# Kernel optimization log

Hardware: AMD Instinct MI355X
Metric: run time of the kernel (lower is better)

## Reference

```python
import jax, jax.numpy as jnp
import numpy as np

EPS = 1e-6
HEADS, HEAD_DIM = 8, 64

def rms_norm_ch(x, g):
    # x: [B,C,H,W], normalize over channel dim, scale g: [C]
    mean = jnp.mean(x * x, axis=1, keepdims=True)
    return x * jax.lax.rsqrt(mean + EPS) * g[None, :, None, None]

def rms_norm_last(x, g):
    # x: [B,L,D], normalize over feature dim, scale g: [D]
    mean = jnp.mean(x * x, axis=-1, keepdims=True)
    return x * jax.lax.rsqrt(mean + EPS) * g

def setup_inputs() -> dict:
    key = jax.random.key(0)
    ks = jax.random.split(key, 5)
    B, C, H, W = 8, 512, 32, 32
    Lc = 1024
    hidden = HEADS * HEAD_DIM  # 512
    x = jax.random.normal(ks[0], (B, C, H, W), dtype=jnp.float32)
    context = jax.random.normal(ks[1], (B, Lc, C), dtype=jnp.float32)
    Wq = jax.random.normal(ks[2], (hidden, C), dtype=jnp.float32) * 0.02
    Wkv = jax.random.normal(ks[3], (2 * hidden, C), dtype=jnp.float32) * 0.02
    Wo = jax.random.normal(ks[4], (C, hidden), dtype=jnp.float32) * 0.02
    bo = jnp.zeros((C,), dtype=jnp.float32)
    g = jnp.ones((C,), dtype=jnp.float32)   # shared RMSNorm scale (pre-attn)
    g2 = jnp.ones((C,), dtype=jnp.float32)  # output RMSNorm scale
    return {"x": x, "context": context, "Wq": Wq, "Wkv": Wkv, "Wo": Wo, "bo": bo, "g": g, "g2": g2}

def reference(x, context, Wq, Wkv, Wo, bo, g, g2):
    B, C, H, W = x.shape
    Lc = context.shape[1]
    hidden = HEADS * HEAD_DIM
    scale = HEAD_DIM ** -0.5

    # Q projection: 1x1 conv == per-pixel matmul
    xn = rms_norm_ch(x, g)
    q = jnp.einsum('oc,bchw->bohw', Wq, xn)                     # [B,hidden,H,W]
    q = q.reshape(B, HEADS, HEAD_DIM, H * W) * scale            # [B,h,d,lw1]

    # K,V from context tokens
    cn = rms_norm_last(context, g)
    kv = jnp.einsum('bld,od->blo', cn, Wkv)                     # [B,Lc,2*hidden]
    k, v = jnp.split(kv, 2, axis=-1)
    k = k.reshape(B, Lc, HEADS, HEAD_DIM).transpose(0, 2, 3, 1)  # [B,h,d,lw2]
    v = v.reshape(B, Lc, HEADS, HEAD_DIM).transpose(0, 2, 3, 1)  # [B,h,d,lw2]

    sim = jnp.einsum('bhci,bhcj->bhij', q, k)                   # [B,h,lw1,lw2]
    attn = jax.nn.softmax(sim, axis=-1)
    out = jnp.einsum('bhij,bhcj->bhic', attn, v)                # [B,h,lw1,d]

    out = out.transpose(0, 1, 3, 2).reshape(B, hidden, H, W)    # b (h c) l w
    y = jnp.einsum('oc,bchw->bohw', Wo, out) + bo[None, :, None, None]
    y = rms_norm_ch(y, g2)
    return y + x
```

## Files before the change

kernel.cpp:

```cpp
#include <hip/hip_runtime.h>
#include <hip/hip_bf16.h>

using bf16 = __hip_bfloat16;
typedef float f32x4 __attribute__((ext_vector_type(4)));
typedef short s16x8 __attribute__((ext_vector_type(8)));
typedef short s16x4 __attribute__((ext_vector_type(4)));

#define B_N   8
#define C_N   512
#define HW_N  1024
#define LC_N  1024
#define HID_N 512
#define NHEAD 8
#define DHEAD 64
#define EPSN  1e-6f

__device__ __forceinline__ f32x4 mfma16(s16x8 a, s16x8 b, f32x4 c) {
  return __builtin_amdgcn_mfma_f32_16x16x32_bf16(a, b, c, 0, 0, 0);
}
__device__ __forceinline__ void gload_lds16(const void* g, void* l) {
  __builtin_amdgcn_global_load_lds((const __attribute__((address_space(1))) void*)g,
                                   (__attribute__((address_space(3))) void*)l, 16, 0, 0);
}
__device__ __forceinline__ s16x8 ld8(const bf16* p) {
  return *reinterpret_cast<const s16x8*>(p);
}
__device__ __forceinline__ unsigned short bfbits(float f) {
  return __builtin_bit_cast(unsigned short, __float2bfloat16(f));
}

__global__ __launch_bounds__(256) void prep_weights(
    const float* __restrict__ Wq, const float* __restrict__ Wkv,
    const float* __restrict__ Wo, const float* __restrict__ g,
    bf16* __restrict__ Wqg, bf16* __restrict__ Wkvg, bf16* __restrict__ Wob,
    float* __restrict__ ssq)
{
  int idx = blockIdx.x * 256 + threadIdx.x;
  const int NQ = 512 * 512, NKV = 1024 * 512;
  if (idx < 8192) ssq[idx] = 0.f;
  if (idx < NQ) {
    Wqg[idx] = __float2bfloat16(Wq[idx] * g[idx & 511]);
  } else if (idx < NQ + NKV) {
    int j = idx - NQ;
    Wkvg[j] = __float2bfloat16(Wkv[j] * g[j & 511]);
  } else {
    int j = idx - NQ - NKV;
    Wob[j] = __float2bfloat16(Wo[j]);
  }
}

__global__ __launch_bounds__(256) void rstd_ch_kernel(
    const float* __restrict__ x, float* __restrict__ rstd)
{
  __shared__ float part[16][16];
  int tp = threadIdx.x & 15, tc = threadIdx.x >> 4;
  int gp = blockIdx.x * 16 + tp;
  int b = gp >> 10, p = gp & 1023;
  const float* xb = x + (long)b * C_N * HW_N + p;
  float s = 0.f;
  for (int c = tc * 32; c < tc * 32 + 32; ++c) {
    float v = xb[(long)c * HW_N];
    s += v * v;
  }
  part[tc][tp] = s;
  __syncthreads();
  if (tc == 0) {
    float tot = 0.f;
#pragma unroll
    for (int i = 0; i < 16; ++i) tot += part[i][tp];
    rstd[gp] = rsqrtf(tot * (1.0f / C_N) + EPSN);
  }
}

__global__ __launch_bounds__(256) void xbf_kernel(
    const float* __restrict__ x, const float* __restrict__ rstd, bf16* __restrict__ xbf)
{
  __shared__ float tile[32][33];
  int b = blockIdx.z, c0 = blockIdx.y * 32, p0 = blockIdx.x * 32;
  int tx = threadIdx.x & 31, ty = threadIdx.x >> 5;
#pragma unroll
  for (int j = 0; j < 4; ++j) {
    int c = ty + j * 8;
    tile[c][tx] = x[((long)b * C_N + c0 + c) * HW_N + p0 + tx];
  }
  __syncthreads();
#pragma unroll
  for (int j = 0; j < 4; ++j) {
    int p = ty + j * 8;
    float r = rstd[b * HW_N + p0 + p];
    xbf[((long)b * HW_N + p0 + p) * C_N + c0 + tx] = __float2bfloat16(tile[tx][p] * r);
  }
}

__global__ __launch_bounds__(256) void ctxnorm_kernel(
    const float* __restrict__ ctx, bf16* __restrict__ cnbf)
{
  int row = blockIdx.x * 4 + (threadIdx.x >> 6);
  int lane = threadIdx.x & 63;
  const float* cr = ctx + (long)row * C_N;
  float4 v0 = ((const float4*)cr)[lane * 2];
  float4 v1 = ((const float4*)cr)[lane * 2 + 1];
  float s = v0.x*v0.x + v0.y*v0.y + v0.z*v0.z + v0.w*v0.w
          + v1.x*v1.x + v1.y*v1.y + v1.z*v1.z + v1.w*v1.w;
#pragma unroll
  for (int m = 1; m < 64; m <<= 1) s += __shfl_xor(s, m);
  float r = rsqrtf(s * (1.0f / C_N) + EPSN);
  bf16 tmp[8];
  tmp[0] = __float2bfloat16(v0.x * r); tmp[1] = __float2bfloat16(v0.y * r);
  tmp[2] = __float2bfloat16(v0.z * r); tmp[3] = __float2bfloat16(v0.w * r);
  tmp[4] = __float2bfloat16(v1.x * r); tmp[5] = __float2bfloat16(v1.y * r);
  tmp[6] = __float2bfloat16(v1.z * r); tmp[7] = __float2bfloat16(v1.w * r);
  *reinterpret_cast<s16x8*>(cnbf + (long)row * C_N + lane * 8) =
      *reinterpret_cast<const s16x8*>(tmp);
}

__device__ __forceinline__ void gemm128_core(
    const bf16* __restrict__ A, const bf16* __restrict__ W, int K, int m0, int n0,
    bf16* __restrict__ sA, bf16* __restrict__ sB, f32x4 (&acc)[4][4])
{
  const int t = threadIdx.x;
  const int lane = t & 63, w = t >> 6;
  const int wm = (w >> 1) * 64, wn = (w & 1) * 64;
  const int lr = lane & 15, hi = lane >> 4;
  const int r = t >> 2, seg = t & 3;
  const long aoff0 = (long)(m0 + r) * K + seg * 8;
  const long aoff1 = (long)(m0 + 64 + r) * K + seg * 8;
  const long woff0 = (long)(n0 + r) * K + seg * 8;
  const long woff1 = (long)(n0 + 64 + r) * K + seg * 8;
  const int d0 = r * 32 + seg * 8, d1 = (64 + r) * 32 + seg * 8;

#define GSTAGE(buf, k0)                                           \
  do {                                                            \
    gload_lds16(A + aoff0 + (k0), &sA[(buf) * 4096 + d0]);        \
    gload_lds16(A + aoff1 + (k0), &sA[(buf) * 4096 + d1]);        \
    gload_lds16(W + woff0 + (k0), &sB[(buf) * 4096 + d0]);        \
    gload_lds16(W + woff1 + (k0), &sB[(buf) * 4096 + d1]);        \
  } while (0)

  GSTAGE(0, 0);
  __syncthreads();
  int cur = 0;
  for (int k0 = 0; k0 < K; k0 += 32) {
    if (k0 + 32 < K) GSTAGE(cur ^ 1, k0 + 32);
    s16x8 af[4], bfr[4];
#pragma unroll
    for (int mi = 0; mi < 4; ++mi)
      af[mi] = *reinterpret_cast<const s16x8*>(
          &sA[cur * 4096 + (wm + mi * 16 + lr) * 32 + hi * 8]);
#pragma unroll
    for (int ni = 0; ni < 4; ++ni)
      bfr[ni] = *reinterpret_cast<const s16x8*>(
          &sB[cur * 4096 + (wn + ni * 16 + lr) * 32 + hi * 8]);
#pragma unroll
    for (int mi = 0; mi < 4; ++mi)
#pragma unroll
      for (int ni = 0; ni < 4; ++ni)
        acc[mi][ni] = mfma16(af[mi], bfr[ni], acc[mi][ni]);
    __syncthreads();
    cur ^= 1;
  }
#undef GSTAGE
}

__global__ __launch_bounds__(256, 2)
void gemm_qkv(const bf16* __restrict__ xbf, const bf16* __restrict__ cnbf,
              const bf16* __restrict__ Wqg, const bf16* __restrict__ Wkvg,
              bf16* __restrict__ qbf, bf16* __restrict__ kvbf, bf16* __restrict__ vT)
{
  __shared__ bf16 sA[2 * 4096];
  __shared__ bf16 sB[2 * 4096];
  const int bid = blockIdx.x;
  const bf16 *A, *W;
  int N, m0, n0;
  bool isQ;
  if (bid < 256) {
    isQ = true;  A = xbf;  W = Wqg;  N = HID_N;
    m0 = (bid >> 2) * 128; n0 = (bid & 3) * 128;
  } else {
    isQ = false; A = cnbf; W = Wkvg; N = 2 * HID_N;
    int b2 = bid - 256;
    m0 = (b2 >> 3) * 128; n0 = (b2 & 7) * 128;
  }
  f32x4 acc[4][4] = {};
  gemm128_core(A, W, C_N, m0, n0, sA, sB, acc);

  const int lane = threadIdx.x & 63, w = threadIdx.x >> 6;
  const int wm = (w >> 1) * 64, wn = (w & 1) * 64;
  const int lr = lane & 15, hi = lane >> 4;
  const float scale = isQ ? 0.18033688011112042f : 1.0f;
#pragma unroll
  for (int mi = 0; mi < 4; ++mi) {
#pragma unroll
    for (int ni = 0; ni < 4; ++ni) {
#pragma unroll
      for (int rr = 0; rr < 4; ++rr) {
        int row = m0 + wm + mi * 16 + hi * 4 + rr;
        int col = n0 + wn + ni * 16 + lr;
        float v = acc[mi][ni][rr] * scale;
        if (isQ) {
          qbf[(long)row * HID_N + col] = __float2bfloat16(v);
        } else if (col < HID_N) {
          kvbf[(long)row * (2 * HID_N) + col] = __float2bfloat16(v);
        } else {
          int b = row >> 10, l = row & 1023;
          vT[((long)b * HID_N + (col - HID_N)) * LC_N + l] = __float2bfloat16(v);
        }
      }
    }
  }
}

__global__ __launch_bounds__(256, 2)
void gemm_o(const bf16* __restrict__ attno, const bf16* __restrict__ Wob,
            const float* __restrict__ bo, float* __restrict__ ytmp,
            float* __restrict__ ssq)
{
  __shared__ bf16 sA[2 * 4096];
  __shared__ bf16 sB[2 * 4096];
  const int m0 = (blockIdx.x >> 2) * 128;
  const int n0 = (blockIdx.x & 3) * 128;
  f32x4 acc[4][4] = {};
  gemm128_core(attno, Wob, HID_N, m0, n0, sA, sB, acc);

  const int lane = threadIdx.x & 63, w = threadIdx.x >> 6;
  const int wm = (w >> 1) * 64, wn = (w & 1) * 64;
  const int lr = lane & 15, hi = lane >> 4;
  float ss[4][4];
#pragma unroll
  for (int mi = 0; mi < 4; ++mi)
#pragma unroll
    for (int rr = 0; rr < 4; ++rr) ss[mi][rr] = 0.f;

#pragma unroll
  for (int mi = 0; mi < 4; ++mi) {
#pragma unroll
    for (int ni = 0; ni < 4; ++ni) {
      float bb = bo[n0 + wn + ni * 16 + lr];
#pragma unroll
      for (int rr = 0; rr < 4; ++rr) {
        int row = m0 + wm + mi * 16 + hi * 4 + rr;
        int col = n0 + wn + ni * 16 + lr;
        float v = acc[mi][ni][rr] + bb;
        ytmp[(long)row * C_N + col] = v;
        ss[mi][rr] += v * v;
      }
    }
  }
#pragma unroll
  for (int mi = 0; mi < 4; ++mi)
#pragma unroll
    for (int rr = 0; rr < 4; ++rr) {
      float s = ss[mi][rr];
      s += __shfl_xor(s, 1); s += __shfl_xor(s, 2);
      s += __shfl_xor(s, 4); s += __shfl_xor(s, 8);
      if (lr == 0) atomicAdd(&ssq[m0 + wm + mi * 16 + hi * 4 + rr], s);
    }
}

__global__ __launch_bounds__(256, 2)
void attn_fused(const bf16* __restrict__ qbf, const bf16* __restrict__ kvbf,
                const bf16* __restrict__ vT, bf16* __restrict__ attno)
{
  __shared__ bf16 sK[2][4096];
  __shared__ bf16 sV[2][4096];
  __shared__ bf16 Pl[4][32 * 72];
  const int t = threadIdx.x;
  const int wv = t >> 6, lane = t & 63;
  const int lr = lane & 15, hi = lane >> 4;
  const int hi8 = hi * 8, hi4 = hi * 4;
  const int bh = blockIdx.x, b = bh >> 3, h = bh & 7;
  const int q_base = blockIdx.y * 128 + wv * 32;

  const bf16* kbase = kvbf + (long)b * LC_N * 1024 + h * DHEAD;
  const bf16* vbase = vT + ((long)b * HID_N + h * DHEAD) * (long)LC_N;
  bf16* Pw = Pl[wv];

  s16x8 qf[2][2];
#pragma unroll
  for (int qt = 0; qt < 2; ++qt)
#pragma unroll
    for (int c = 0; c < 2; ++c)
      qf[qt][c] = ld8(qbf + ((long)b * HW_N + q_base + qt * 16 + lr) * HID_N
                          + h * DHEAD + c * 32 + hi8);

  const int srow = lane >> 2;
  const int scol = (lane & 3) * 8;

#define ASTAGE(buf, l0n)                                                        \
  do {                                                                          \
    _Pragma("unroll")                                                           \
    for (int j = 0; j < 4; ++j) {                                               \
      int lin = wv * 4 + j;                                                     \
      int cc = (lin >> 2) & 1, qq = lin & 3;                                    \
      if (lin < 8) {                                                            \
        gload_lds16(kbase + (long)((l0n) + qq * 16 + srow) * 1024 + cc * 32 + scol, \
                    &sK[buf][cc * 2048 + qq * 512 + lane * 8]);                 \
      } else {                                                                  \
        gload_lds16(vbase + (long)(qq * 16 + srow) * 1024 + (l0n) + cc * 32 + scol, \
                    &sV[buf][cc * 2048 + qq * 512 + lane * 8]);                 \
      }                                                                         \
    }                                                                           \
  } while (0)

  float m[2] = {-1e30f, -1e30f};
  float lsum[2] = {0.f, 0.f};
  f32x4 o[2][4] = {};

  ASTAGE(0, 0);
  __syncthreads();
  int cur = 0;

#pragma unroll 1
  for (int l0 = 0; l0 < LC_N; l0 += 64) {
    if (l0 + 64 < LC_N) ASTAGE(cur ^ 1, l0 + 64);

    f32x4 st[4][2] = {};
#pragma unroll
    for (int kt = 0; kt < 4; ++kt) {
      s16x8 k0 = *reinterpret_cast<const s16x8*>(&sK[cur][(kt * 16 + lr) * 32 + hi8]);
      s16x8 k1 = *reinterpret_cast<const s16x8*>(&sK[cur][2048 + (kt * 16 + lr) * 32 + hi8]);
      st[kt][0] = mfma16(k0, qf[0][0], st[kt][0]);
      st[kt][0] = mfma16(k1, qf[0][1], st[kt][0]);
      st[kt][1] = mfma16(k0, qf[1][0], st[kt][1]);
      st[kt][1] = mfma16(k1, qf[1][1], st[kt][1]);
    }

    float pmax[2];
#pragma unroll
    for (int qt = 0; qt < 2; ++qt) {
      float mx = st[0][qt][0];
#pragma unroll
      for (int kt = 0; kt < 4; ++kt)
#pragma unroll
        for (int rr = 0; rr < 4; ++rr)
          mx = fmaxf(mx, st[kt][qt][rr]);
      pmax[qt] = mx;
    }
    bool ok = (pmax[0] <= m[0] + 8.f) && (pmax[1] <= m[1] + 8.f);
    if (!__all(ok)) {
#pragma unroll
      for (int qt = 0; qt < 2; ++qt) {
        float rm = pmax[qt];
        rm = fmaxf(rm, __shfl_xor(rm, 16));
        rm = fmaxf(rm, __shfl_xor(rm, 32));
        float mn = fmaxf(m[qt], rm);
        float al = __builtin_amdgcn_exp2f(m[qt] - mn);
        m[qt] = mn;
        lsum[qt] *= al;
        float arr[4];
#pragma unroll
        for (int rr = 0; rr < 4; ++rr) arr[rr] = __shfl(al, hi4 + rr);
#pragma unroll
        for (int dt = 0; dt < 4; ++dt)
#pragma unroll
          for (int rr = 0; rr < 4; ++rr) o[qt][dt][rr] *= arr[rr];
      }
    }

#pragma unroll
    for (int qt = 0; qt < 2; ++qt) {
      float ls = 0.f;
#pragma unroll
      for (int kt = 0; kt < 4; ++kt) {
        float p0 = __builtin_amdgcn_exp2f(st[kt][qt][0] - m[qt]);
        float p1 = __builtin_amdgcn_exp2f(st[kt][qt][1] - m[qt]);
        float p2 = __builtin_amdgcn_exp2f(st[kt][qt][2] - m[qt]);
        float p3 = __builtin_amdgcn_exp2f(st[kt][qt][3] - m[qt]);
        ls += (p0 + p1) + (p2 + p3);
        s16x4 pk;
        pk[0] = (short)bfbits(p0); pk[1] = (short)bfbits(p1);
        pk[2] = (short)bfbits(p2); pk[3] = (short)bfbits(p3);
        *reinterpret_cast<s16x4*>(&Pw[(qt * 16 + lr) * 72 + kt * 16 + hi4]) = pk;
      }
      lsum[qt] += ls;
    }

#pragma unroll
    for (int c = 0; c < 2; ++c) {
      s16x8 pa0 = *reinterpret_cast<const s16x8*>(&Pw[(0 * 16 + lr) * 72 + c * 32 + hi8]);
      s16x8 pa1 = *reinterpret_cast<const s16x8*>(&Pw[(1 * 16 + lr) * 72 + c * 32 + hi8]);
#pragma unroll
      for (int dt = 0; dt < 4; ++dt) {
        s16x8 vv = *reinterpret_cast<const s16x8*>(
            &sV[cur][c * 2048 + (dt * 16 + lr) * 32 + hi8]);
        o[0][dt] = mfma16(pa0, vv, o[0][dt]);
        o[1][dt] = mfma16(pa1, vv, o[1][dt]);
      }
    }

    __syncthreads();
    cur ^= 1;
  }
#undef ASTAGE

#pragma unroll
  for (int qt = 0; qt < 2; ++qt) {
    float ls = lsum[qt];
    ls += __shfl_xor(ls, 16);
    ls += __shfl_xor(ls, 32);
    float linv[4];
#pragma unroll
    for (int rr = 0; rr < 4; ++rr) linv[rr] = 1.f / __shfl(ls, hi4 + rr);
#pragma unroll
    for (int dt = 0; dt < 4; ++dt)
#pragma unroll
      for (int rr = 0; rr < 4; ++rr)
        attno[((long)b * HW_N + q_base + qt * 16 + hi4 + rr) * HID_N
              + h * DHEAD + dt * 16 + lr] = __float2bfloat16(o[qt][dt][rr] * linv[rr]);
  }
}

__global__ __launch_bounds__(256) void final_kernel(
    const float* __restrict__ ytmp, const float* __restrict__ g2,
    const float* __restrict__ ssq, const float* __restrict__ x,
    float* __restrict__ out)
{
  __shared__ float tile[32][33];
  int b = blockIdx.z, c0 = blockIdx.y * 32, p0 = blockIdx.x * 32;
  int tx = threadIdx.x & 31, ty = threadIdx.x >> 5;
#pragma unroll
  for (int j = 0; j < 4; ++j) {
    int p = ty + j * 8;
    tile[p][tx] = ytmp[((long)b * HW_N + p0 + p) * C_N + c0 + tx];
  }
  __syncthreads();
  float r = rsqrtf(ssq[b * HW_N + p0 + tx] * (1.0f / C_N) + EPSN);
#pragma unroll
  for (int j = 0; j < 4; ++j) {
    int c = ty + j * 8;
    long oidx = ((long)b * C_N + c0 + c) * HW_N + p0 + tx;
    out[oidx] = tile[tx][c] * r * g2[c0 + c] + x[oidx];
  }
}

extern "C" void kernel_launch(void* const* d_in, const int* in_sizes, int n_in,
                              void* d_out, int out_size, void* d_ws, size_t ws_size,
                              hipStream_t stream) {
  const float* x   = (const float*)d_in[0];
  const float* ctx = (const float*)d_in[1];
  const float* Wq  = (const float*)d_in[2];
  const float* Wkv = (const float*)d_in[3];
  const float* Wo  = (const float*)d_in[4];
  const float* bo  = (const float*)d_in[5];
  const float* g   = (const float*)d_in[6];
  const float* g2  = (const float*)d_in[7];
  float* out = (float*)d_out;

  char* ws = (char*)d_ws;
  bf16*  Wqg   = (bf16*)(ws + 0);
  bf16*  Wkvg  = (bf16*)(ws + 524288);
  bf16*  Wob   = (bf16*)(ws + 1572864);
  float* rstdx = (float*)(ws + 2097152);
  float* ssq   = (float*)(ws + 2129920);
  bf16*  xbf   = (bf16*)(ws + 2162688);
  bf16*  cnbf  = (bf16*)(ws + 10551296);
  bf16*  qbf   = (bf16*)(ws + 18939904);
  bf16*  kvbf  = (bf16*)(ws + 27328512);
  bf16*  vT    = (bf16*)(ws + 44105728);
  bf16*  attno = (bf16*)(ws + 52494336);
  float* ytmp  = (float*)(ws + 2162688);

  prep_weights<<<4096, 256, 0, stream>>>(Wq, Wkv, Wo, g, Wqg, Wkvg, Wob, ssq);
  rstd_ch_kernel<<<512, 256, 0, stream>>>(x, rstdx);
  xbf_kernel<<<dim3(32, 16, 8), 256, 0, stream>>>(x, rstdx, xbf);
  ctxnorm_kernel<<<2048, 256, 0, stream>>>(ctx, cnbf);

  gemm_qkv<<<768, 256, 0, stream>>>(xbf, cnbf, Wqg, Wkvg, qbf, kvbf, vT);

  attn_fused<<<dim3(64, 8), 256, 0, stream>>>(qbf, kvbf, vT, attno);

  gemm_o<<<256, 256, 0, stream>>>(attno, Wob, bo, ytmp, ssq);

  final_kernel<<<dim3(32, 16, 8), 256, 0, stream>>>(ytmp, g2, ssq, x, out);
}
```

Before: 193.3 us.

## Fold x RMS-norm into Q GEMM epilogue and raise MFMA wave priority

Removes the separate rstd_ch pass over x. xbf_kernel now writes unnormalized bf16 x and accumulates per-pixel sum of squares with atomics. The Q GEMM epilogue then applies rsqrt scaling per row, which is valid because the per-pixel norm factors out of the linear projection. This saves one full read of x (16 MB) and one launch, at the cost of atomics and bf16 rounding before normalization. It also adds s_setprio around the MFMA blocks in the GEMM core and the attention kernel to favour matrix issue across waves.

```diff
diff --git a/kernel.cpp b/kernel.cpp
--- a/kernel.cpp
+++ b/kernel.cpp
@@ -33,11 +33,11 @@
     const float* __restrict__ Wq, const float* __restrict__ Wkv,
     const float* __restrict__ Wo, const float* __restrict__ g,
     bf16* __restrict__ Wqg, bf16* __restrict__ Wkvg, bf16* __restrict__ Wob,
-    float* __restrict__ ssq)
+    float* __restrict__ ssqx, float* __restrict__ ssqy)
 {
   int idx = blockIdx.x * 256 + threadIdx.x;
   const int NQ = 512 * 512, NKV = 1024 * 512;
-  if (idx < 8192) ssq[idx] = 0.f;
+  if (idx < 8192) { ssqx[idx] = 0.f; ssqy[idx] = 0.f; }
   if (idx < NQ) {
     Wqg[idx] = __float2bfloat16(Wq[idx] * g[idx & 511]);
   } else if (idx < NQ + NKV) {
@@ -49,33 +49,11 @@
   }
 }
 
-__global__ __launch_bounds__(256) void rstd_ch_kernel(
-    const float* __restrict__ x, float* __restrict__ rstd)
-{
-  __shared__ float part[16][16];
-  int tp = threadIdx.x & 15, tc = threadIdx.x >> 4;
-  int gp = blockIdx.x * 16 + tp;
-  int b = gp >> 10, p = gp & 1023;
-  const float* xb = x + (long)b * C_N * HW_N + p;
-  float s = 0.f;
-  for (int c = tc * 32; c < tc * 32 + 32; ++c) {
-    float v = xb[(long)c * HW_N];
-    s += v * v;
-  }
-  part[tc][tp] = s;
-  __syncthreads();
-  if (tc == 0) {
-    float tot = 0.f;
-#pragma unroll
-    for (int i = 0; i < 16; ++i) tot += part[i][tp];
-    rstd[gp] = rsqrtf(tot * (1.0f / C_N) + EPSN);
-  }
-}
-
 __global__ __launch_bounds__(256) void xbf_kernel(
-    const float* __restrict__ x, const float* __restrict__ rstd, bf16* __restrict__ xbf)
+    const float* __restrict__ x, bf16* __restrict__ xbf, float* __restrict__ ssqx)
 {
   __shared__ float tile[32][33];
+  __shared__ float part[8][32];
   int b = blockIdx.z, c0 = blockIdx.y * 32, p0 = blockIdx.x * 32;
   int tx = threadIdx.x & 31, ty = threadIdx.x >> 5;
 #pragma unroll
@@ -84,11 +62,26 @@
     tile[c][tx] = x[((long)b * C_N + c0 + c) * HW_N + p0 + tx];
   }
   __syncthreads();
+  {
+    float s = 0.f;
+#pragma unroll
+    for (int i = 0; i < 4; ++i) {
+      float v = tile[ty * 4 + i][tx];
+      s += v * v;
+    }
+    part[ty][tx] = s;
+  }
 #pragma unroll
   for (int j = 0; j < 4; ++j) {
     int p = ty + j * 8;
-    float r = rstd[b * HW_N + p0 + p];
-    xbf[((long)b * HW_N + p0 + p) * C_N + c0 + tx] = __float2bfloat16(tile[tx][p] * r);
+    xbf[((long)b * HW_N + p0 + p) * C_N + c0 + tx] = __float2bfloat16(tile[tx][p]);
+  }
+  __syncthreads();
+  if (ty == 0) {
+    float tot = 0.f;
+#pragma unroll
+    for (int i = 0; i < 8; ++i) tot += part[i][tx];
+    atomicAdd(&ssqx[b * HW_N + p0 + tx], tot);
   }
 }
 
@@ -151,11 +144,13 @@
     for (int ni = 0; ni < 4; ++ni)
       bfr[ni] = *reinterpret_cast<const s16x8*>(
           &sB[cur * 4096 + (wn + ni * 16 + lr) * 32 + hi * 8]);
+    __builtin_amdgcn_s_setprio(1);
 #pragma unroll
     for (int mi = 0; mi < 4; ++mi)
 #pragma unroll
       for (int ni = 0; ni < 4; ++ni)
         acc[mi][ni] = mfma16(af[mi], bfr[ni], acc[mi][ni]);
+    __builtin_amdgcn_s_setprio(0);
     __syncthreads();
     cur ^= 1;
   }
@@ -165,19 +160,20 @@
 __global__ __launch_bounds__(256, 2)
 void gemm_qkv(const bf16* __restrict__ xbf, const bf16* __restrict__ cnbf,
               const bf16* __restrict__ Wqg, const bf16* __restrict__ Wkvg,
+              const float* __restrict__ ssqx,
               bf16* __restrict__ qbf, bf16* __restrict__ kvbf, bf16* __restrict__ vT)
 {
   __shared__ bf16 sA[2 * 4096];
   __shared__ bf16 sB[2 * 4096];
   const int bid = blockIdx.x;
   const bf16 *A, *W;
-  int N, m0, n0;
+  int m0, n0;
   bool isQ;
   if (bid < 256) {
-    isQ = true;  A = xbf;  W = Wqg;  N = HID_N;
+    isQ = true;  A = xbf;  W = Wqg;
     m0 = (bid >> 2) * 128; n0 = (bid & 3) * 128;
   } else {
-    isQ = false; A = cnbf; W = Wkvg; N = 2 * HID_N;
+    isQ = false; A = cnbf; W = Wkvg;
     int b2 = bid - 256;
     m0 = (b2 >> 3) * 128; n0 = (b2 & 7) * 128;
   }
@@ -187,18 +183,20 @@
   const int lane = threadIdx.x & 63, w = threadIdx.x >> 6;
   const int wm = (w >> 1) * 64, wn = (w & 1) * 64;
   const int lr = lane & 15, hi = lane >> 4;
-  const float scale = isQ ? 0.18033688011112042f : 1.0f;
 #pragma unroll
   for (int mi = 0; mi < 4; ++mi) {
 #pragma unroll
-    for (int ni = 0; ni < 4; ++ni) {
-#pragma unroll
-      for (int rr = 0; rr < 4; ++rr) {
-        int row = m0 + wm + mi * 16 + hi * 4 + rr;
+    for (int rr = 0; rr < 4; ++rr) {
+      int row = m0 + wm + mi * 16 + hi * 4 + rr;
+      float rsc = 0.f;
+      if (isQ)
+        rsc = rsqrtf(ssqx[row] * (1.0f / C_N) + EPSN) * 0.18033688011112042f;
+#pragma unroll
+      for (int ni = 0; ni < 4; ++ni) {
         int col = n0 + wn + ni * 16 + lr;
-        float v = acc[mi][ni][rr] * scale;
+        float v = acc[mi][ni][rr];
         if (isQ) {
-          qbf[(long)row * HID_N + col] = __float2bfloat16(v);
+          qbf[(long)row * HID_N + col] = __float2bfloat16(v * rsc);
         } else if (col < HID_N) {
           kvbf[(long)row * (2 * HID_N) + col] = __float2bfloat16(v);
         } else {
@@ -213,7 +211,7 @@
 __global__ __launch_bounds__(256, 2)
 void gemm_o(const bf16* __restrict__ attno, const bf16* __restrict__ Wob,
             const float* __restrict__ bo, float* __restrict__ ytmp,
-            float* __restrict__ ssq)
+            float* __restrict__ ssqy)
 {
   __shared__ bf16 sA[2 * 4096];
   __shared__ bf16 sB[2 * 4096];
@@ -253,7 +251,7 @@
       float s = ss[mi][rr];
       s += __shfl_xor(s, 1); s += __shfl_xor(s, 2);
       s += __shfl_xor(s, 4); s += __shfl_xor(s, 8);
-      if (lr == 0) atomicAdd(&ssq[m0 + wm + mi * 16 + hi * 4 + rr], s);
+      if (lr == 0) atomicAdd(&ssqy[m0 + wm + mi * 16 + hi * 4 + rr], s);
     }
 }
 
@@ -315,6 +313,7 @@
     if (l0 + 64 < LC_N) ASTAGE(cur ^ 1, l0 + 64);
 
     f32x4 st[4][2] = {};
+    __builtin_amdgcn_s_setprio(1);
 #pragma unroll
     for (int kt = 0; kt < 4; ++kt) {
       s16x8 k0 = *reinterpret_cast<const s16x8*>(&sK[cur][(kt * 16 + lr) * 32 + hi8]);
@@ -324,6 +323,7 @@
       st[kt][1] = mfma16(k0, qf[1][0], st[kt][1]);
       st[kt][1] = mfma16(k1, qf[1][1], st[kt][1]);
     }
+    __builtin_amdgcn_s_setprio(0);
 
     float pmax[2];
 #pragma unroll
@@ -375,6 +375,7 @@
       lsum[qt] += ls;
     }
 
+    __builtin_amdgcn_s_setprio(1);
 #pragma unroll
     for (int c = 0; c < 2; ++c) {
       s16x8 pa0 = *reinterpret_cast<const s16x8*>(&Pw[(0 * 16 + lr) * 72 + c * 32 + hi8]);
@@ -387,6 +388,7 @@
         o[1][dt] = mfma16(pa1, vv, o[1][dt]);
       }
     }
+    __builtin_amdgcn_s_setprio(0);
 
     __syncthreads();
     cur ^= 1;
@@ -412,7 +414,7 @@
 
 __global__ __launch_bounds__(256) void final_kernel(
     const float* __restrict__ ytmp, const float* __restrict__ g2,
-    const float* __restrict__ ssq, const float* __restrict__ x,
+    const float* __restrict__ ssqy, const float* __restrict__ x,
     float* __restrict__ out)
 {
   __shared__ float tile[32][33];
@@ -424,7 +426,7 @@
     tile[p][tx] = ytmp[((long)b * HW_N + p0 + p) * C_N + c0 + tx];
   }
   __syncthreads();
-  float r = rsqrtf(ssq[b * HW_N + p0 + tx] * (1.0f / C_N) + EPSN);
+  float r = rsqrtf(ssqy[b * HW_N + p0 + tx] * (1.0f / C_N) + EPSN);
 #pragma unroll
   for (int j = 0; j < 4; ++j) {
     int c = ty + j * 8;
@@ -450,8 +452,8 @@
   bf16*  Wqg   = (bf16*)(ws + 0);
   bf16*  Wkvg  = (bf16*)(ws + 524288);
   bf16*  Wob   = (bf16*)(ws + 1572864);
-  float* rstdx = (float*)(ws + 2097152);
-  float* ssq   = (float*)(ws + 2129920);
+  float* ssqx  = (float*)(ws + 2097152);
+  float* ssqy  = (float*)(ws + 2129920);
   bf16*  xbf   = (bf16*)(ws + 2162688);
   bf16*  cnbf  = (bf16*)(ws + 10551296);
   bf16*  qbf   = (bf16*)(ws + 18939904);
@@ -460,16 +462,15 @@
   bf16*  attno = (bf16*)(ws + 52494336);
   float* ytmp  = (float*)(ws + 2162688);
 
-  prep_weights<<<4096, 256, 0, stream>>>(Wq, Wkv, Wo, g, Wqg, Wkvg, Wob, ssq);
-  rstd_ch_kernel<<<512, 256, 0, stream>>>(x, rstdx);
-  xbf_kernel<<<dim3(32, 16, 8), 256, 0, stream>>>(x, rstdx, xbf);
+  prep_weights<<<4096, 256, 0, stream>>>(Wq, Wkv, Wo, g, Wqg, Wkvg, Wob, ssqx, ssqy);
+  xbf_kernel<<<dim3(32, 16, 8), 256, 0, stream>>>(x, xbf, ssqx);
   ctxnorm_kernel<<<2048, 256, 0, stream>>>(ctx, cnbf);
 
-  gemm_qkv<<<768, 256, 0, stream>>>(xbf, cnbf, Wqg, Wkvg, qbf, kvbf, vT);
+  gemm_qkv<<<768, 256, 0, stream>>>(xbf, cnbf, Wqg, Wkvg, ssqx, qbf, kvbf, vT);
 
   attn_fused<<<dim3(64, 8), 256, 0, stream>>>(qbf, kvbf, vT, attno);
 
-  gemm_o<<<256, 256, 0, stream>>>(attno, Wob, bo, ytmp, ssq);
-
-  final_kernel<<<dim3(32, 16, 8), 256, 0, stream>>>(ytmp, g2, ssq, x, out);
-}
+  gemm_o<<<256, 256, 0, stream>>>(attno, Wob, bo, ytmp, ssqy);
+
+  final_kernel<<<dim3(32, 16, 8), 256, 0, stream>>>(ytmp, g2, ssqy, x, out);
+}
```

After: 184.9 us. -4.3%, faster.
